# Optimization experiments

Hardware: AMD Instinct MI355X
Metric: run time of the kernel (lower is better)

## Reference

```python
import jax, jax.numpy as jnp
import numpy as np

HEADS = 8
DIM_HEAD = 64
DIM = 512
B, N = 4, 2048
SCALE = DIM_HEAD ** -0.5


def setup_inputs() -> dict:
    key = jax.random.key(0)
    k1, k2, k3, k4, k5, k6 = jax.random.split(key, 6)
    inner = HEADS * DIM_HEAD
    s = DIM ** -0.5
    return {
        "input_feature": jax.random.normal(k1, (B, N, DIM), dtype=jnp.float32),
        "mask": jax.random.randint(k2, (B, N), 0, 2, dtype=jnp.int32),
        "Wq": jax.random.normal(k3, (inner, DIM), dtype=jnp.float32) * s,
        "Wk": jax.random.normal(k4, (inner, DIM), dtype=jnp.float32) * s,
        "Wv": jax.random.normal(k5, (inner, DIM), dtype=jnp.float32) * s,
        "Wout": jax.random.normal(k6, (DIM, inner), dtype=jnp.float32) * s,
    }


def reference(input_feature, mask, Wq, Wk, Wv, Wout):
    # Conv1d with kernel_size=1, no bias == per-token linear: out = W @ x_channels
    q = jnp.einsum('bnc,dc->bnd', input_feature, Wq)  # [B, N, H*Dh]
    k = jnp.einsum('bnc,dc->bnd', input_feature, Wk)
    v = jnp.einsum('bnc,dc->bnd', input_feature, Wv)

    # '(n c)' channel layout is head-major -> reshape to [B, N, H, Dh], move head out front
    def split_heads(t):
        return t.reshape(B, N, HEADS, DIM_HEAD).transpose(2, 0, 1, 3)  # [H, B, N, Dh]

    q, k, v = split_heads(q), split_heads(k), split_heads(v)

    scores = jnp.einsum('hbtd,hbsd->hbts', q, k) * SCALE  # [H, B, N, N]
    # masked_fill(mask == 0, 1e-9): fill with small CONSTANT (not -inf), faithful to source
    m = (mask == 0)[None, :, None, :]  # [1, B, 1, N]
    scores = jnp.where(m, jnp.float32(1e-9), scores)
    att = jax.nn.softmax(scores, axis=-1)
    out = jnp.einsum('hbts,hbsd->hbtd', att, v)  # [H, B, N, Dh]

    # '(n b) tokens c -> b (n c) tokens' : head-major channel concat
    out = out.transpose(1, 2, 0, 3).reshape(B, N, HEADS * DIM_HEAD)  # [B, N, H*Dh]
    out = jnp.einsum('bnd,ed->bne', out, Wout)  # [B, N, DIM]
    return out
```

## Files before the change

### kernel.cpp

```cpp
#include <hip/hip_runtime.h>
#include <hip/hip_bf16.h>

typedef __attribute__((ext_vector_type(8))) short short8;
typedef __attribute__((ext_vector_type(4))) short short4_t;
typedef __attribute__((ext_vector_type(4))) float float4_;

#define LOG2E 1.4426950408889634f

__device__ __forceinline__ short f2bf(float f) {
    unsigned int u = __builtin_bit_cast(unsigned int, f);
    u = (u + 0x7FFFu + ((u >> 16) & 1u)) >> 16;
    return (short)u;
}

__device__ __forceinline__ unsigned pk2bf(float a, float b) {
    unsigned ua = __builtin_bit_cast(unsigned, a) + 0x8000u;
    unsigned ub = __builtin_bit_cast(unsigned, b) + 0x8000u;
    return __builtin_amdgcn_perm(ub, ua, 0x07060302);
}

__device__ __forceinline__ void gload_lds16(const short* g, short* l) {
    __builtin_amdgcn_global_load_lds((const __attribute__((address_space(1))) void*)g,
                                     (__attribute__((address_space(3))) void*)l, 16, 0, 0);
}

__global__ __launch_bounds__(256) void cvt_kernel(
    const float* __restrict__ X, const float* __restrict__ Wq, const float* __restrict__ Wk,
    const float* __restrict__ Wv, const float* __restrict__ Wo,
    short* __restrict__ Xb, short* __restrict__ Wqkvb, short* __restrict__ Wob) {
    int i = blockIdx.x * 256 + threadIdx.x;
    const float* src; short* dst; float sc = 1.0f;
    if (i < 1048576) { src = X + (size_t)i * 4; dst = Xb + (size_t)i * 4; }
    else {
        int w = i - 1048576; int sec = w >> 16; int j = (w & 65535) * 4;
        if (sec == 0)      { src = Wq + j; dst = Wqkvb + j; sc = 0.125f * LOG2E; }
        else if (sec == 1) { src = Wk + j; dst = Wqkvb + 262144 + j; }
        else if (sec == 2) { src = Wv + j; dst = Wqkvb + 524288 + j; }
        else               { src = Wo + j; dst = Wob + j; }
    }
    float4 v = *(const float4*)src;
    short4_t o;
    o[0] = f2bf(v.x * sc); o[1] = f2bf(v.y * sc); o[2] = f2bf(v.z * sc); o[3] = f2bf(v.w * sc);
    *(short4_t*)dst = o;
}

__global__ __launch_bounds__(256) void gemm_qkv(const short* __restrict__ A, const short* __restrict__ B,
                                                const int* __restrict__ mask,
                                                short* __restrict__ Qb, short* __restrict__ Kb,
                                                short* __restrict__ Vtb) {
    __shared__ short At[128 * 64];
    __shared__ short Bt[128 * 64];
    __shared__ int maskL[128];
    constexpr int K = 512;
    int tid = threadIdx.x;
    int wid = tid >> 6, lane = tid & 63;
    int quad = lane >> 4, cc = lane & 15;
    int c7 = cc & 7;
    int wr = wid >> 1, wc = wid & 1;
    int m0 = blockIdx.y * 128, n0 = blockIdx.x * 128;
    if (tid < 128) maskL[tid] = mask[m0 + tid];

    float4_ acc[4][4] = {};

    for (int kk = 0; kk < K; kk += 64) {
#pragma unroll
        for (int p = 0; p < 4; ++p) {
            int slot = p * 256 + tid;
            int r = slot >> 3, c = slot & 7;
            int cs = (c ^ (r & 7)) * 8;
            gload_lds16(A + (size_t)(m0 + r) * K + kk + cs, At + slot * 8);
            gload_lds16(B + (size_t)(n0 + r) * K + kk + cs, Bt + slot * 8);
        }
        __syncthreads();
#pragma unroll
        for (int kc = 0; kc < 2; ++kc) {
            short8 af[4], bf[4];
#pragma unroll
            for (int i = 0; i < 4; ++i)
                af[i] = *(const short8*)(At + (wr * 64 + i * 16 + cc) * 64 + (((kc * 4 + quad) ^ c7) * 8));
#pragma unroll
            for (int j = 0; j < 4; ++j)
                bf[j] = *(const short8*)(Bt + (wc * 64 + j * 16 + cc) * 64 + (((kc * 4 + quad) ^ c7) * 8));
#pragma unroll
            for (int i = 0; i < 4; ++i)
#pragma unroll
                for (int j = 0; j < 4; ++j)
                    acc[i][j] = __builtin_amdgcn_mfma_f32_16x16x32_bf16(af[i], bf[j], acc[i][j], 0, 0, 0);
        }
        __syncthreads();
    }

    int which = n0 >> 9;
    int b = m0 >> 11;
    if (which == 2) {
#pragma unroll
        for (int i = 0; i < 4; ++i) {
#pragma unroll
            for (int j = 0; j < 4; ++j) {
                int d = (n0 & 511) + wc * 64 + j * 16 + cc;
                int nn = (m0 & 2047) + wr * 64 + i * 16 + quad * 4;
                short4_t pv;
                pv[0] = f2bf(acc[i][j][0]); pv[1] = f2bf(acc[i][j][1]);
                pv[2] = f2bf(acc[i][j][2]); pv[3] = f2bf(acc[i][j][3]);
                *(short4_t*)(Vtb + ((size_t)(b * 512 + d)) * 2048 + nn) = pv;
            }
        }
    } else {
        short* dst = which ? Kb : Qb;
#pragma unroll
        for (int i = 0; i < 4; ++i) {
#pragma unroll
            for (int j = 0; j < 4; ++j) {
#pragma unroll
                for (int r = 0; r < 4; ++r) {
                    int lm = wr * 64 + i * 16 + quad * 4 + r;
                    int nn = (m0 & 2047) + lm;
                    int hd = (n0 & 511) + wc * 64 + j * 16 + cc;
                    int h = hd >> 6, dh = hd & 63;
                    float v = acc[i][j][r];
                    if (which == 1 && maskL[lm] == 0) v = 0.0f;
                    dst[((((size_t)b * 8 + h) * 2048 + nn) * 64) + dh] = f2bf(v);
                }
            }
        }
    }
}

__global__ __launch_bounds__(256, 4) void attn_kernel(const short* __restrict__ Q, const short* __restrict__ Kg,
                                                      const short* __restrict__ Vt,
                                                      short* __restrict__ AO) {
    __shared__ __align__(16) char smem[40960];
    short* KbufL = (short*)smem;
    short* VbufL = (short*)(smem + 16384);
    short* Pt    = (short*)(smem + 32768);
    float* Lw    = (float*)smem;
    float* Lfin  = (float*)(smem + 1024);

    int tid = threadIdx.x;
    int w = tid >> 6, lane = tid & 63;
    int quad = lane >> 4, cc = lane & 15;
    int tg = w >> 1, dh = w & 1;
    int bh = blockIdx.x, b = bh >> 3, h = bh & 7;
    int t0 = blockIdx.y * 64;
    size_t kbase = (size_t)bh * 2048 * 64;
    size_t vbase = (size_t)b * 512 * 2048 + (size_t)h * 64 * 2048;

    short8 qf[4][2];
#pragma unroll
    for (int tb = 0; tb < 4; ++tb)
#pragma unroll
        for (int kc = 0; kc < 2; ++kc)
            qf[tb][kc] = *(const short8*)(Q + kbase + (size_t)(t0 + tb * 16 + cc) * 64 + kc * 32 + quad * 8);

    int c7 = cc & 7;
    int koff[2], poff_w[4], aoff[2][2], voff[2][2];
#pragma unroll
    for (int kc = 0; kc < 2; ++kc)
        koff[kc] = (w * 16 + cc) * 64 + (((kc * 4 + quad) ^ c7) * 8);
#pragma unroll
    for (int tb = 0; tb < 4; ++tb)
        poff_w[tb] = (tb * 16 + cc) * 64 + (((w * 2 + (quad >> 1)) ^ c7) * 8) + (quad & 1) * 4;
#pragma unroll
    for (int mb = 0; mb < 2; ++mb)
#pragma unroll
        for (int kc = 0; kc < 2; ++kc)
            aoff[mb][kc] = (tg * 32 + mb * 16 + cc) * 64 + (((kc * 4 + quad) ^ c7) * 8);
#pragma unroll
    for (int db = 0; db < 2; ++db)
#pragma unroll
        for (int kc = 0; kc < 2; ++kc)
            voff[db][kc] = (dh * 32 + db * 16 + cc) * 64 + (((kc * 4 + quad) ^ c7) * 8);

    float4_ o[2][2] = {};
    float lp[4] = {0.f, 0.f, 0.f, 0.f};

    int sA = tid >> 3, cA = tid & 7;
    const short* gK0 = Kg + kbase + (size_t)sA * 64 + ((cA ^ (sA & 7)) * 8);
    const short* gK1 = gK0 + 32 * 64;
    const short* gV0 = Vt + vbase + (size_t)sA * 2048 + ((cA ^ (sA & 7)) * 8);
    const short* gV1 = gV0 + 32 * 2048;
    int ld0 = tid * 8, ld1 = tid * 8 + 2048;

    short8 krg0 = *(const short8*)gK0, krg1 = *(const short8*)gK1;
    short8 vrg0 = *(const short8*)gV0, vrg1 = *(const short8*)gV1;
    gK0 += 4096; gK1 += 4096; gV0 += 64; gV1 += 64;
    *(short8*)(KbufL + ld0) = krg0; *(short8*)(KbufL + ld1) = krg1;
    *(short8*)(VbufL + ld0) = vrg0; *(short8*)(VbufL + ld1) = vrg1;
    krg0 = *(const short8*)gK0; krg1 = *(const short8*)gK1;
    vrg0 = *(const short8*)gV0; vrg1 = *(const short8*)gV1;
    gK0 += 4096; gK1 += 4096; gV0 += 64; gV1 += 64;

    for (int it = 0; it < 32; ++it) {
        int cur = it & 1;
        const short* Kt  = KbufL + cur * 4096;
        const short* Vtt = VbufL + cur * 4096;
        __syncthreads();

        if (it < 31) {
            short* Kn = KbufL + (cur ^ 1) * 4096;
            short* Vn = VbufL + (cur ^ 1) * 4096;
            *(short8*)(Kn + ld0) = krg0; *(short8*)(Kn + ld1) = krg1;
            *(short8*)(Vn + ld0) = vrg0; *(short8*)(Vn + ld1) = vrg1;
        }
        if (it < 30) {
            krg0 = *(const short8*)gK0; krg1 = *(const short8*)gK1;
            vrg0 = *(const short8*)gV0; vrg1 = *(const short8*)gV1;
            gK0 += 4096; gK1 += 4096; gV0 += 64; gV1 += 64;
        }

        short8 kf0 = *(const short8*)(Kt + koff[0]);
        short8 kf1 = *(const short8*)(Kt + koff[1]);
        float4_ acc[4];
#pragma unroll
        for (int tb = 0; tb < 4; ++tb) {
            float4_ a = {0.f, 0.f, 0.f, 0.f};
            a = __builtin_amdgcn_mfma_f32_16x16x32_bf16(kf0, qf[tb][0], a, 0, 0, 0);
            a = __builtin_amdgcn_mfma_f32_16x16x32_bf16(kf1, qf[tb][1], a, 0, 0, 0);
            acc[tb] = a;
        }
#pragma unroll
        for (int tb = 0; tb < 4; ++tb) {
            float x0 = __builtin_amdgcn_exp2f(acc[tb][0]);
            float x1 = __builtin_amdgcn_exp2f(acc[tb][1]);
            float x2 = __builtin_amdgcn_exp2f(acc[tb][2]);
            float x3 = __builtin_amdgcn_exp2f(acc[tb][3]);
            lp[tb] += (x0 + x1) + (x2 + x3);
            uint2 pw; pw.x = pk2bf(x0, x1); pw.y = pk2bf(x2, x3);
            *(uint2*)(Pt + poff_w[tb]) = pw;
        }
        __syncthreads();

        short8 af[2][2], vf[2][2];
#pragma unroll
        for (int mb = 0; mb < 2; ++mb)
#pragma unroll
            for (int kc = 0; kc < 2; ++kc)
                af[mb][kc] = *(const short8*)(Pt + aoff[mb][kc]);
#pragma unroll
        for (int db = 0; db < 2; ++db)
#pragma unroll
            for (int kc = 0; kc < 2; ++kc)
                vf[db][kc] = *(const short8*)(Vtt + voff[db][kc]);
#pragma unroll
        for (int mb = 0; mb < 2; ++mb)
#pragma unroll
            for (int db = 0; db < 2; ++db) {
                o[mb][db] = __builtin_amdgcn_mfma_f32_16x16x32_bf16(af[mb][0], vf[db][0], o[mb][db], 0, 0, 0);
                o[mb][db] = __builtin_amdgcn_mfma_f32_16x16x32_bf16(af[mb][1], vf[db][1], o[mb][db], 0, 0, 0);
            }
    }

#pragma unroll
    for (int tb = 0; tb < 4; ++tb) {
        lp[tb] += __shfl_xor(lp[tb], 16, 64);
        lp[tb] += __shfl_xor(lp[tb], 32, 64);
    }
    __syncthreads();
    if (lane < 16) {
#pragma unroll
        for (int tb = 0; tb < 4; ++tb) Lw[w * 64 + tb * 16 + lane] = lp[tb];
    }
    __syncthreads();
    if (tid < 64) {
        float s = Lw[tid] + Lw[64 + tid] + Lw[128 + tid] + Lw[192 + tid];
        Lfin[tid] = 1.0f / s;
    }
    __syncthreads();

#pragma unroll
    for (int mb = 0; mb < 2; ++mb)
#pragma unroll
        for (int r = 0; r < 4; ++r) {
            int tl = tg * 32 + mb * 16 + quad * 4 + r;
            float inv = Lfin[tl];
            size_t rowbase = ((size_t)(b * 2048 + t0 + tl)) * 512 + h * 64;
#pragma unroll
            for (int db = 0; db < 2; ++db)
                AO[rowbase + dh * 32 + db * 16 + cc] = f2bf(o[mb][db][r] * inv);
        }
}

__global__ __launch_bounds__(256) void gemm_out(const short* __restrict__ A, const short* __restrict__ B,
                                                float* __restrict__ C) {
    __shared__ short At[64 * 64];
    __shared__ short Bt[64 * 64];
    constexpr int K = 512;
    int tid = threadIdx.x;
    int wid = tid >> 6, lane = tid & 63;
    int quad = lane >> 4, cc = lane & 15;
    int c7 = cc & 7;
    int wr = wid >> 1, wc = wid & 1;
    int m0 = blockIdx.y * 64, n0 = blockIdx.x * 64;

    float4_ acc[2][2] = {};

    for (int kk = 0; kk < K; kk += 64) {
#pragma unroll
        for (int p = 0; p < 2; ++p) {
            int slot = p * 256 + tid;
            int r = slot >> 3, c = slot & 7;
            int cs = (c ^ (r & 7)) * 8;
            gload_lds16(A + (size_t)(m0 + r) * K + kk + cs, At + slot * 8);
            gload_lds16(B + (size_t)(n0 + r) * K + kk + cs, Bt + slot * 8);
        }
        __syncthreads();
#pragma unroll
        for (int kc = 0; kc < 2; ++kc) {
            short8 af[2], bf[2];
#pragma unroll
            for (int i = 0; i < 2; ++i)
                af[i] = *(const short8*)(At + (wr * 32 + i * 16 + cc) * 64 + (((kc * 4 + quad) ^ c7) * 8));
#pragma unroll
            for (int j = 0; j < 2; ++j)
                bf[j] = *(const short8*)(Bt + (wc * 32 + j * 16 + cc) * 64 + (((kc * 4 + quad) ^ c7) * 8));
#pragma unroll
            for (int i = 0; i < 2; ++i)
#pragma unroll
                for (int j = 0; j < 2; ++j)
                    acc[i][j] = __builtin_amdgcn_mfma_f32_16x16x32_bf16(af[i], bf[j], acc[i][j], 0, 0, 0);
        }
        __syncthreads();
    }

#pragma unroll
    for (int i = 0; i < 2; ++i)
#pragma unroll
        for (int j = 0; j < 2; ++j)
#pragma unroll
            for (int r = 0; r < 4; ++r) {
                int gm = m0 + wr * 32 + i * 16 + quad * 4 + r;
                int gn = n0 + wc * 32 + j * 16 + cc;
                C[(size_t)gm * 512 + gn] = acc[i][j][r];
            }
}

extern "C" void kernel_launch(void* const* d_in, const int* in_sizes, int n_in,
                              void* d_out, int out_size, void* d_ws, size_t ws_size,
                              hipStream_t stream) {
    const float* X  = (const float*)d_in[0];
    const int* mask = (const int*)d_in[1];
    const float* Wq = (const float*)d_in[2];
    const float* Wk = (const float*)d_in[3];
    const float* Wv = (const float*)d_in[4];
    const float* Wo = (const float*)d_in[5];

    char* ws = (char*)d_ws;
    short* Xbf   = (short*)(ws + 0);
    short* Wqkvb = (short*)(ws + 8388608);
    short* Wob   = (short*)(ws + 9961472);
    short* Qb    = (short*)(ws + 10485760);
    short* Kb    = (short*)(ws + 18874368);
    short* Vtb   = (short*)(ws + 27262976);
    short* AOb   = (short*)(ws + 35651584);

    cvt_kernel<<<5120, 256, 0, stream>>>(X, Wq, Wk, Wv, Wo, Xbf, Wqkvb, Wob);
    gemm_qkv<<<dim3(12, 64), 256, 0, stream>>>(Xbf, Wqkvb, mask, Qb, Kb, Vtb);
    attn_kernel<<<dim3(32, 32), 256, 0, stream>>>(Qb, Kb, Vtb, AOb);
    gemm_out<<<dim3(8, 128), 256, 0, stream>>>(AOb, Wob, (float*)d_out);
}
```

Baseline: 166.4 us.

## Register-prefetch QKV GEMM tiles and stage V-transpose stores through LDS

```diff
diff --git a/kernel.cpp b/kernel.cpp
--- a/kernel.cpp
+++ b/kernel.cpp
@@ -48,9 +48,10 @@
                                                 const int* __restrict__ mask,
                                                 short* __restrict__ Qb, short* __restrict__ Kb,
                                                 short* __restrict__ Vtb) {
-    __shared__ short At[128 * 64];
-    __shared__ short Bt[128 * 64];
+    __shared__ __align__(16) short smemAB[2 * 8192];
     __shared__ int maskL[128];
+    short* At = smemAB;
+    short* Bt = smemAB + 8192;
     constexpr int K = 512;
     int tid = threadIdx.x;
     int wid = tid >> 6, lane = tid & 63;
@@ -60,16 +61,35 @@
     int m0 = blockIdx.y * 128, n0 = blockIdx.x * 128;
     if (tid < 128) maskL[tid] = mask[m0 + tid];
 
+    const short* gA[4]; const short* gB[4]; int lofs[4];
+#pragma unroll
+    for (int p = 0; p < 4; ++p) {
+        int slot = p * 256 + tid;
+        int r = slot >> 3, c = slot & 7;
+        int cs = (c ^ (r & 7)) * 8;
+        gA[p] = A + (size_t)(m0 + r) * K + cs;
+        gB[p] = B + (size_t)(n0 + r) * K + cs;
+        lofs[p] = slot * 8;
+    }
+    short8 arg[4], brg[4];
+#pragma unroll
+    for (int p = 0; p < 4; ++p) { arg[p] = *(const short8*)gA[p]; brg[p] = *(const short8*)gB[p]; }
+
     float4_ acc[4][4] = {};
 
     for (int kk = 0; kk < K; kk += 64) {
+        __syncthreads();
 #pragma unroll
         for (int p = 0; p < 4; ++p) {
-            int slot = p * 256 + tid;
-            int r = slot >> 3, c = slot & 7;
-            int cs = (c ^ (r & 7)) * 8;
-            gload_lds16(A + (size_t)(m0 + r) * K + kk + cs, At + slot * 8);
-            gload_lds16(B + (size_t)(n0 + r) * K + kk + cs, Bt + slot * 8);
+            *(short8*)(At + lofs[p]) = arg[p];
+            *(short8*)(Bt + lofs[p]) = brg[p];
+        }
+        if (kk < K - 64) {
+#pragma unroll
+            for (int p = 0; p < 4; ++p) {
+                arg[p] = *(const short8*)(gA[p] + kk + 64);
+                brg[p] = *(const short8*)(gB[p] + kk + 64);
+            }
         }
         __syncthreads();
 #pragma unroll
@@ -87,23 +107,34 @@
                 for (int j = 0; j < 4; ++j)
                     acc[i][j] = __builtin_amdgcn_mfma_f32_16x16x32_bf16(af[i], bf[j], acc[i][j], 0, 0, 0);
         }
-        __syncthreads();
     }
 
     int which = n0 >> 9;
     int b = m0 >> 11;
     if (which == 2) {
+        __syncthreads();
+        short* T = smemAB;
 #pragma unroll
         for (int i = 0; i < 4; ++i) {
 #pragma unroll
             for (int j = 0; j < 4; ++j) {
-                int d = (n0 & 511) + wc * 64 + j * 16 + cc;
-                int nn = (m0 & 2047) + wr * 64 + i * 16 + quad * 4;
+                int d_l = wc * 64 + j * 16 + cc;
+                int nnb = wr * 64 + i * 16 + quad * 4;
+                int G = nnb >> 3, half = (nnb >> 2) & 1;
+                int Gs = G ^ (d_l & 15);
                 short4_t pv;
                 pv[0] = f2bf(acc[i][j][0]); pv[1] = f2bf(acc[i][j][1]);
                 pv[2] = f2bf(acc[i][j][2]); pv[3] = f2bf(acc[i][j][3]);
-                *(short4_t*)(Vtb + ((size_t)(b * 512 + d)) * 2048 + nn) = pv;
-            }
+                *(short4_t*)(T + d_l * 128 + Gs * 8 + half * 4) = pv;
+            }
+        }
+        __syncthreads();
+#pragma unroll
+        for (int p = 0; p < 8; ++p) {
+            int slot = p * 256 + tid;
+            int d = slot >> 4, G = slot & 15;
+            short8 v = *(const short8*)(T + d * 128 + ((G ^ (d & 15)) * 8));
+            *(short8*)(Vtb + ((size_t)(b * 512 + (n0 & 511) + d)) * 2048 + (m0 & 2047) + G * 8) = v;
         }
     } else {
         short* dst = which ? Kb : Qb;
```

New measurement: 165.4 us. No clear change (-0.6%).
